# Kernel tuning notes

Measured on AMD Instinct MI355X. Metric: run time of the kernel, lower is better.

The kernel has to match this reference:

```python
import jax, jax.numpy as jnp
import numpy as np

N, M, E = 100000, 50000, 1600000
C_IN, C_OUT = 128, 128
BN_EPS = 1e-5


def setup_inputs() -> dict:
    key = jax.random.key(0)
    ks = jax.random.split(key, 10)
    ref_bxyz = jax.random.normal(ks[0], (N, 4), dtype=jnp.float32)
    ref_feat = jax.random.normal(ks[1], (N, C_IN), dtype=jnp.float32)
    query_bxyz = jax.random.normal(ks[2], (M, 4), dtype=jnp.float32)
    e_ref = jax.random.randint(ks[3], (E,), 0, N)
    e_query = jax.random.randint(ks[4], (E,), 0, M)
    # pos_encoder: Linear(3, C_OUT); mlp: Linear(C_IN, C_OUT); BatchNorm1d(C_OUT)
    W_pos = jax.random.normal(ks[5], (C_OUT, 3), dtype=jnp.float32) / np.sqrt(3.0)
    b_pos = jnp.zeros((C_OUT,), dtype=jnp.float32)
    W_mlp = jax.random.normal(ks[6], (C_OUT, C_IN), dtype=jnp.float32) / np.sqrt(C_IN)
    b_mlp = jnp.zeros((C_OUT,), dtype=jnp.float32)
    gamma = jnp.ones((C_OUT,), dtype=jnp.float32)
    beta = jnp.zeros((C_OUT,), dtype=jnp.float32)
    return {
        "ref_bxyz": ref_bxyz, "ref_feat": ref_feat, "query_bxyz": query_bxyz,
        "e_ref": e_ref, "e_query": e_query,
        "W_pos": W_pos, "b_pos": b_pos, "W_mlp": W_mlp, "b_mlp": b_mlp,
        "gamma": gamma, "beta": beta,
    }


def reference(ref_bxyz, ref_feat, query_bxyz, e_ref, e_query,
              W_pos, b_pos, W_mlp, b_mlp, gamma, beta):
    num_q = query_bxyz.shape[0]
    # gather endpoints, xyz difference (drop batch-index column 0)
    pos_diff = (ref_bxyz[e_ref] - query_bxyz[e_query])[:, 1:4]          # [E, 3]
    pos_embedding = pos_diff @ W_pos.T + b_pos                           # [E, C_OUT]
    output_feat = (ref_feat @ W_mlp.T + b_mlp)[e_ref]                   # [E, C_OUT]
    # scatter-mean into queries (empty segments -> 0, clamp count at 1)
    s = jax.ops.segment_sum(pos_embedding + output_feat, e_query, num_segments=num_q)
    cnt = jax.ops.segment_sum(jnp.ones((e_query.shape[0],), pos_embedding.dtype),
                              e_query, num_segments=num_q)
    query_feat = s / jnp.maximum(cnt, 1.0)[:, None]                     # [M, C_OUT]
    # BatchNorm1d (training-mode batch stats, biased variance) + ReLU
    mu = jnp.mean(query_feat, axis=0)
    var = jnp.mean(jnp.square(query_feat - mu), axis=0)
    normed = (query_feat - mu) * jax.lax.rsqrt(var + BN_EPS) * gamma + beta
    return jax.nn.relu(normed)
```

## Files before the change

### kernel.cpp

```cpp
#include <hip/hip_runtime.h>


__device__ __forceinline__ float bf_lo(unsigned u) {
  union { unsigned u; float f; } c; c.u = u << 16; return c.f;
}
__device__ __forceinline__ float bf_hi(unsigned u) {
  union { unsigned u; float f; } c; c.u = u & 0xFFFF0000u; return c.f;
}
__device__ __forceinline__ unsigned pack_bf(float x, float y) {
  union { float f; unsigned u; } a, b; a.f = x; b.f = y;
  unsigned lo = (a.u + 0x7FFFu + ((a.u >> 16) & 1u)) >> 16;
  unsigned hi = (b.u + 0x7FFFu + ((b.u >> 16) & 1u)) >> 16;
  return lo | (hi << 16);
}

__global__ __launch_bounds__(256) void k_build_cvt(
    const int* __restrict__ eq, const int* __restrict__ er,
    int* __restrict__ head, int2* __restrict__ node,
    const float4* __restrict__ featf, uint4* __restrict__ featb,
    int E_, int n8) {
  int i = blockIdx.x * blockDim.x + threadIdx.x;
  if (i < n8) {
    float4 a = featf[2 * i], b = featf[2 * i + 1];
    uint4 o;
    o.x = pack_bf(a.x, a.y);
    o.y = pack_bf(a.z, a.w);
    o.z = pack_bf(b.x, b.y);
    o.w = pack_bf(b.z, b.w);
    featb[i] = o;
  }
  if (i < E_) {
    int q = eq[i];
    int prev = atomicExch(&head[q], i);
    node[i] = make_int2(prev, er[i]);
  }
}

__global__ __launch_bounds__(256) void k_accum_b(const int* __restrict__ head,
                                                 const int2* __restrict__ node,
                                                 const uint4* __restrict__ featb,
                                                 const float* __restrict__ bxyz,
                                                 float4* __restrict__ accF4,
                                                 float* __restrict__ possum, int M_) {
  int q = blockIdx.x * 16 + (threadIdx.x >> 4);
  int l = threadIdx.x & 15;
  if (q >= M_) return;
  int i = head[q];
  float a0 = 0.f, a1 = 0.f, a2 = 0.f, a3 = 0.f;
  float a4 = 0.f, a5 = 0.f, a6 = 0.f, a7 = 0.f;
  float p = 0.f, c = 0.f;
  while (i >= 0) {
    int2 nd = node[i];
    int r = nd.y;
    uint4 v = featb[(size_t)r * 16 + l];
    a0 += bf_lo(v.x); a1 += bf_hi(v.x);
    a2 += bf_lo(v.y); a3 += bf_hi(v.y);
    a4 += bf_lo(v.z); a5 += bf_hi(v.z);
    a6 += bf_lo(v.w); a7 += bf_hi(v.w);
    if (l < 3) p += bxyz[r * 4 + 1 + l];
    c += 1.f;
    i = nd.x;
  }
  float4 o0 = make_float4(a0, a1, a2, a3);
  float4 o1 = make_float4(a4, a5, a6, a7);
  accF4[(size_t)q * 32 + l * 2] = o0;
  accF4[(size_t)q * 32 + l * 2 + 1] = o1;
  if (l < 3) possum[q * 4 + l] = p;
  if (l == 3) possum[q * 4 + 3] = c;
}

__global__ __launch_bounds__(256) void k_gemm(
    const float* __restrict__ accF, const float4* __restrict__ possum4,
    const float* __restrict__ qxyz,
    const float* __restrict__ Wm, const float* __restrict__ Wp,
    const float* __restrict__ bm, const float* __restrict__ bp,
    float* __restrict__ out, float* __restrict__ stats, int M_) {
  __shared__ float sA[32 * 132];
  __shared__ float sW[128 * 34];
  int t = threadIdx.x;
  int q0 = blockIdx.x * 32;
  #pragma unroll
  for (int i = 0; i < 4; ++i) {
    int f = t + 256 * i;
    int q = f >> 5;
    int kk = (f & 31) << 2;
    float4 v = make_float4(0.f, 0.f, 0.f, 0.f);
    if (q0 + q < M_) v = *(const float4*)&accF[(q0 + q) * 128 + kk];
    *(float4*)&sA[q * 132 + kk] = v;
  }
  float acc[4][4];
  #pragma unroll
  for (int i = 0; i < 4; ++i)
    #pragma unroll
    for (int j = 0; j < 4; ++j) acc[i][j] = 0.f;
  int q0l = (t >> 5) << 2;
  int cb = t & 31;
  float2* sW2 = (float2*)sW;
  const float2* Wm2 = (const float2*)Wm;
  for (int kt = 0; kt < 4; ++kt) {
    __syncthreads();
    #pragma unroll
    for (int i = 0; i < 8; ++i) {
      int f = t + 256 * i;
      int c = f >> 4;
      int kk2 = f & 15;
      sW2[c * 17 + kk2] = Wm2[c * 64 + kt * 16 + kk2];
    }
    __syncthreads();
    #pragma unroll
    for (int kk4 = 0; kk4 < 8; ++kk4) {
      float4 av[4];
      float2 wa[4], wb[4];
      #pragma unroll
      for (int i = 0; i < 4; ++i)
        av[i] = *(const float4*)&sA[(q0l + i) * 132 + kt * 32 + (kk4 << 2)];
      #pragma unroll
      for (int j = 0; j < 4; ++j) {
        int c = cb + 32 * j;
        wa[j] = sW2[c * 17 + kk4 * 2];
        wb[j] = sW2[c * 17 + kk4 * 2 + 1];
      }
      #pragma unroll
      for (int i = 0; i < 4; ++i)
        #pragma unroll
        for (int j = 0; j < 4; ++j) {
          acc[i][j] = fmaf(av[i].x, wa[j].x, acc[i][j]);
          acc[i][j] = fmaf(av[i].y, wa[j].y, acc[i][j]);
          acc[i][j] = fmaf(av[i].z, wb[j].x, acc[i][j]);
          acc[i][j] = fmaf(av[i].w, wb[j].y, acc[i][j]);
        }
    }
  }
  float fcnt[4], inv[4], dx[4], dy[4], dz[4];
  #pragma unroll
  for (int i = 0; i < 4; ++i) {
    int q = q0 + q0l + i;
    if (q < M_) {
      float4 ps = possum4[q];
      float fc = ps.w;
      fcnt[i] = fc;
      inv[i] = 1.f / fmaxf(fc, 1.f);
      dx[i] = ps.x - fc * qxyz[q * 4 + 1];
      dy[i] = ps.y - fc * qxyz[q * 4 + 2];
      dz[i] = ps.z - fc * qxyz[q * 4 + 3];
    } else {
      fcnt[i] = 0.f; inv[i] = 1.f; dx[i] = dy[i] = dz[i] = 0.f;
    }
  }
  float psum[4], psq[4];
  #pragma unroll
  for (int j = 0; j < 4; ++j) {
    int c = cb + 32 * j;
    float w0 = Wp[c * 3 + 0], w1 = Wp[c * 3 + 1], w2 = Wp[c * 3 + 2];
    float bb = bm[c] + bp[c];
    float s = 0.f, s2 = 0.f;
    #pragma unroll
    for (int i = 0; i < 4; ++i) {
      int q = q0 + q0l + i;
      float v = acc[i][j] + dx[i] * w0 + dy[i] * w1 + dz[i] * w2 + fcnt[i] * bb;
      float val = v * inv[i];
      if (q >= M_) val = 0.f;
      if (q < M_) out[q * 128 + c] = val;
      s += val; s2 += val * val;
    }
    psum[j] = s; psq[j] = s2;
  }
  __syncthreads();
  float* red = sA;
  int rg = t >> 5;
  #pragma unroll
  for (int j = 0; j < 4; ++j) {
    int c = cb + 32 * j;
    red[c * 8 + rg] = psum[j];
    red[1024 + c * 8 + rg] = psq[j];
  }
  __syncthreads();
  if (t < 128) {
    float s = 0.f, s2 = 0.f;
    #pragma unroll
    for (int r = 0; r < 8; ++r) {
      s += red[t * 8 + r];
      s2 += red[1024 + t * 8 + r];
    }
    atomicAdd(&stats[t], s);
    atomicAdd(&stats[128 + t], s2);
  }
}

__global__ __launch_bounds__(256) void k_bnapply(float* __restrict__ out,
                                                 const float* __restrict__ stats,
                                                 const float* __restrict__ gamma,
                                                 const float* __restrict__ beta,
                                                 float inv_m, int total4) {
  __shared__ float sc[128], sh[128];
  int t = threadIdx.x;
  if (t < 128) {
    float mu = stats[t] * inv_m;
    float var = stats[128 + t] * inv_m - mu * mu;
    var = fmaxf(var, 0.f);
    float s = gamma[t] * rsqrtf(var + 1e-5f);
    sc[t] = s;
    sh[t] = beta[t] - mu * s;
  }
  __syncthreads();
  const float4* sc4 = (const float4*)sc;
  const float4* sh4 = (const float4*)sh;
  float4* o4 = (float4*)out;
  for (int i = blockIdx.x * blockDim.x + t; i < total4;
       i += gridDim.x * blockDim.x) {
    float4 v = o4[i];
    float4 s = sc4[i & 31];
    float4 h = sh4[i & 31];
    v.x = fmaxf(fmaf(v.x, s.x, h.x), 0.f);
    v.y = fmaxf(fmaf(v.y, s.y, h.y), 0.f);
    v.z = fmaxf(fmaf(v.z, s.z, h.z), 0.f);
    v.w = fmaxf(fmaf(v.w, s.w, h.w), 0.f);
    o4[i] = v;
  }
}

static inline size_t align256(size_t x) { return (x + 255) & ~(size_t)255; }

extern "C" void kernel_launch(void* const* d_in, const int* in_sizes, int n_in,
                              void* d_out, int out_size, void* d_ws, size_t ws_size,
                              hipStream_t stream) {
  const float* ref_bxyz   = (const float*)d_in[0];
  const float* ref_feat   = (const float*)d_in[1];
  const float* query_bxyz = (const float*)d_in[2];
  const int*   e_ref      = (const int*)d_in[3];
  const int*   e_query    = (const int*)d_in[4];
  const float* W_pos      = (const float*)d_in[5];
  const float* b_pos      = (const float*)d_in[6];
  const float* W_mlp      = (const float*)d_in[7];
  const float* b_mlp      = (const float*)d_in[8];
  const float* gamma      = (const float*)d_in[9];
  const float* beta       = (const float*)d_in[10];

  int N_ = in_sizes[0] / 4;
  int M_ = in_sizes[2] / 4;
  int E_ = in_sizes[3];

  char* ws = (char*)d_ws;
  size_t off = 0;
  int*   head   = (int*)(ws + off);   off += align256((size_t)M_ * 4);
  int2*  node   = (int2*)(ws + off);  off += align256((size_t)E_ * 8);
  float* possum = (float*)(ws + off); off += align256((size_t)M_ * 4 * 4);
  float* accF   = (float*)(ws + off); off += align256((size_t)M_ * 128 * 4);
  float* stats  = (float*)(ws + off); off += align256(2 * 128 * 4);
  uint4* featb  = (uint4*)(ws + off);

  hipMemsetAsync(head, 0xFF, (size_t)M_ * 4, stream);
  hipMemsetAsync(stats, 0, 2 * 128 * 4, stream);

  float* out = (float*)d_out;
  int n8 = N_ * 16;
  int nwork = (E_ > n8) ? E_ : n8;

  k_build_cvt<<<(nwork + 255) / 256, 256, 0, stream>>>(
      e_query, e_ref, head, node, (const float4*)ref_feat, featb, E_, n8);
  k_accum_b<<<(M_ + 15) / 16, 256, 0, stream>>>(head, node, featb, ref_bxyz,
                                                (float4*)accF, possum, M_);
  k_gemm<<<(M_ + 31) / 32, 256, 0, stream>>>(accF, (const float4*)possum, query_bxyz,
                                             W_mlp, W_pos, b_mlp, b_pos, out, stats, M_);
  k_bnapply<<<2048, 256, 0, stream>>>(out, stats, gamma, beta, 1.f / (float)M_,
                                      M_ * 32);
}
```

Baseline: 353.1 us.

## Fuse gather-accumulate into GEMM kernel, keeping sums in shared memory

Merges the per-query linked-list gather/accumulate kernel into the GEMM kernel, so each block accumulates its 32 queries directly into shared memory instead of writing and re-reading a 25 MB fp32 accumulator buffer. Each half-wave walks two query lists at once to expose more memory-level parallelism. The stats memset moves into the build kernel, and the BN-apply grid is halved. The cost is GEMM work serialized behind irregular list walks within a block, plus a higher occupancy target from launch_bounds(256,4).

```diff
diff --git a/kernel.cpp b/kernel.cpp
--- a/kernel.cpp
+++ b/kernel.cpp
@@ -18,8 +18,9 @@
     const int* __restrict__ eq, const int* __restrict__ er,
     int* __restrict__ head, int2* __restrict__ node,
     const float4* __restrict__ featf, uint4* __restrict__ featb,
-    int E_, int n8) {
+    float* __restrict__ stats, int E_, int n8) {
   int i = blockIdx.x * blockDim.x + threadIdx.x;
+  if (i < 256) stats[i] = 0.f;
   if (i < n8) {
     float4 a = featf[2 * i], b = featf[2 * i + 1];
     uint4 o;
@@ -36,58 +37,55 @@
   }
 }
 
-__global__ __launch_bounds__(256) void k_accum_b(const int* __restrict__ head,
-                                                 const int2* __restrict__ node,
-                                                 const uint4* __restrict__ featb,
-                                                 const float* __restrict__ bxyz,
-                                                 float4* __restrict__ accF4,
-                                                 float* __restrict__ possum, int M_) {
-  int q = blockIdx.x * 16 + (threadIdx.x >> 4);
-  int l = threadIdx.x & 15;
-  if (q >= M_) return;
-  int i = head[q];
-  float a0 = 0.f, a1 = 0.f, a2 = 0.f, a3 = 0.f;
-  float a4 = 0.f, a5 = 0.f, a6 = 0.f, a7 = 0.f;
-  float p = 0.f, c = 0.f;
-  while (i >= 0) {
-    int2 nd = node[i];
-    int r = nd.y;
-    uint4 v = featb[(size_t)r * 16 + l];
-    a0 += bf_lo(v.x); a1 += bf_hi(v.x);
-    a2 += bf_lo(v.y); a3 += bf_hi(v.y);
-    a4 += bf_lo(v.z); a5 += bf_hi(v.z);
-    a6 += bf_lo(v.w); a7 += bf_hi(v.w);
-    if (l < 3) p += bxyz[r * 4 + 1 + l];
-    c += 1.f;
-    i = nd.x;
-  }
-  float4 o0 = make_float4(a0, a1, a2, a3);
-  float4 o1 = make_float4(a4, a5, a6, a7);
-  accF4[(size_t)q * 32 + l * 2] = o0;
-  accF4[(size_t)q * 32 + l * 2 + 1] = o1;
-  if (l < 3) possum[q * 4 + l] = p;
-  if (l == 3) possum[q * 4 + 3] = c;
-}
-
-__global__ __launch_bounds__(256) void k_gemm(
-    const float* __restrict__ accF, const float4* __restrict__ possum4,
+__global__ __launch_bounds__(256, 4) void k_fused(
+    const int* __restrict__ head, const int2* __restrict__ node,
+    const uint4* __restrict__ featb, const float* __restrict__ bxyz,
     const float* __restrict__ qxyz,
     const float* __restrict__ Wm, const float* __restrict__ Wp,
     const float* __restrict__ bm, const float* __restrict__ bp,
     float* __restrict__ out, float* __restrict__ stats, int M_) {
   __shared__ float sA[32 * 132];
   __shared__ float sW[128 * 34];
+  __shared__ float sPS[32][4];
   int t = threadIdx.x;
   int q0 = blockIdx.x * 32;
-  #pragma unroll
-  for (int i = 0; i < 4; ++i) {
-    int f = t + 256 * i;
-    int q = f >> 5;
-    int kk = (f & 31) << 2;
-    float4 v = make_float4(0.f, 0.f, 0.f, 0.f);
-    if (q0 + q < M_) v = *(const float4*)&accF[(q0 + q) * 128 + kk];
-    *(float4*)&sA[q * 132 + kk] = v;
-  }
+  int hw = t >> 4, l = t & 15;
+
+  {
+    int qa = q0 + hw, qb = q0 + hw + 16;
+    int ia = (qa < M_) ? head[qa] : -1;
+    int ib = (qb < M_) ? head[qb] : -1;
+    float aA0=0.f,aA1=0.f,aA2=0.f,aA3=0.f,aA4=0.f,aA5=0.f,aA6=0.f,aA7=0.f;
+    float aB0=0.f,aB1=0.f,aB2=0.f,aB3=0.f,aB4=0.f,aB5=0.f,aB6=0.f,aB7=0.f;
+    float pA=0.f,cA=0.f,pB=0.f,cB=0.f;
+    while (ia >= 0 || ib >= 0) {
+      bool da = ia >= 0, db = ib >= 0;
+      int2 na, nb; uint4 va, vb;
+      if (da) na = node[ia];
+      if (db) nb = node[ib];
+      if (da) va = featb[(size_t)na.y * 16 + l];
+      if (db) vb = featb[(size_t)nb.y * 16 + l];
+      if (da) {
+        aA0+=bf_lo(va.x); aA1+=bf_hi(va.x); aA2+=bf_lo(va.y); aA3+=bf_hi(va.y);
+        aA4+=bf_lo(va.z); aA5+=bf_hi(va.z); aA6+=bf_lo(va.w); aA7+=bf_hi(va.w);
+        if (l < 3) pA += bxyz[na.y * 4 + 1 + l];
+        cA += 1.f; ia = na.x;
+      }
+      if (db) {
+        aB0+=bf_lo(vb.x); aB1+=bf_hi(vb.x); aB2+=bf_lo(vb.y); aB3+=bf_hi(vb.y);
+        aB4+=bf_lo(vb.z); aB5+=bf_hi(vb.z); aB6+=bf_lo(vb.w); aB7+=bf_hi(vb.w);
+        if (l < 3) pB += bxyz[nb.y * 4 + 1 + l];
+        cB += 1.f; ib = nb.x;
+      }
+    }
+    *(float4*)&sA[hw * 132 + 8 * l]          = make_float4(aA0,aA1,aA2,aA3);
+    *(float4*)&sA[hw * 132 + 8 * l + 4]      = make_float4(aA4,aA5,aA6,aA7);
+    *(float4*)&sA[(hw + 16) * 132 + 8 * l]     = make_float4(aB0,aB1,aB2,aB3);
+    *(float4*)&sA[(hw + 16) * 132 + 8 * l + 4] = make_float4(aB4,aB5,aB6,aB7);
+    if (l < 3) { sPS[hw][l] = pA; sPS[hw + 16][l] = pB; }
+    if (l == 3) { sPS[hw][3] = cA; sPS[hw + 16][3] = cB; }
+  }
+
   float acc[4][4];
   #pragma unroll
   for (int i = 0; i < 4; ++i)
@@ -134,15 +132,15 @@
   float fcnt[4], inv[4], dx[4], dy[4], dz[4];
   #pragma unroll
   for (int i = 0; i < 4; ++i) {
-    int q = q0 + q0l + i;
+    int row = q0l + i;
+    int q = q0 + row;
     if (q < M_) {
-      float4 ps = possum4[q];
-      float fc = ps.w;
+      float fc = sPS[row][3];
       fcnt[i] = fc;
       inv[i] = 1.f / fmaxf(fc, 1.f);
-      dx[i] = ps.x - fc * qxyz[q * 4 + 1];
-      dy[i] = ps.y - fc * qxyz[q * 4 + 2];
-      dz[i] = ps.z - fc * qxyz[q * 4 + 3];
+      dx[i] = sPS[row][0] - fc * qxyz[q * 4 + 1];
+      dy[i] = sPS[row][1] - fc * qxyz[q * 4 + 2];
+      dz[i] = sPS[row][2] - fc * qxyz[q * 4 + 3];
     } else {
       fcnt[i] = 0.f; inv[i] = 1.f; dx[i] = dy[i] = dz[i] = 0.f;
     }
@@ -244,24 +242,20 @@
   size_t off = 0;
   int*   head   = (int*)(ws + off);   off += align256((size_t)M_ * 4);
   int2*  node   = (int2*)(ws + off);  off += align256((size_t)E_ * 8);
-  float* possum = (float*)(ws + off); off += align256((size_t)M_ * 4 * 4);
-  float* accF   = (float*)(ws + off); off += align256((size_t)M_ * 128 * 4);
   float* stats  = (float*)(ws + off); off += align256(2 * 128 * 4);
   uint4* featb  = (uint4*)(ws + off);
 
   hipMemsetAsync(head, 0xFF, (size_t)M_ * 4, stream);
-  hipMemsetAsync(stats, 0, 2 * 128 * 4, stream);
 
   float* out = (float*)d_out;
   int n8 = N_ * 16;
   int nwork = (E_ > n8) ? E_ : n8;
 
   k_build_cvt<<<(nwork + 255) / 256, 256, 0, stream>>>(
-      e_query, e_ref, head, node, (const float4*)ref_feat, featb, E_, n8);
-  k_accum_b<<<(M_ + 15) / 16, 256, 0, stream>>>(head, node, featb, ref_bxyz,
-                                                (float4*)accF, possum, M_);
-  k_gemm<<<(M_ + 31) / 32, 256, 0, stream>>>(accF, (const float4*)possum, query_bxyz,
-                                             W_mlp, W_pos, b_mlp, b_pos, out, stats, M_);
-  k_bnapply<<<2048, 256, 0, stream>>>(out, stats, gamma, beta, 1.f / (float)M_,
+      e_query, e_ref, head, node, (const float4*)ref_feat, featb, stats, E_, n8);
+  k_fused<<<(M_ + 31) / 32, 256, 0, stream>>>(head, node, featb, ref_bxyz,
+                                              query_bxyz, W_mlp, W_pos, b_mlp,
+                                              b_pos, out, stats, M_);
+  k_bnapply<<<1024, 256, 0, stream>>>(out, stats, gamma, beta, 1.f / (float)M_,
                                       M_ * 32);
 }
```

After: 396.4 us. +12.3%, slower.

## Fuse pipeline into one cooperative persistent kernel with grid syncs

Applied to the files above, without the earlier changes.

Replaces the two memsets and four separate kernel launches with a single cooperative kernel. The kernel runs the init, bf16 conversion and linked-list build, gather-accumulate, GEMM with BN stats, and BN apply as phases separated by grid.sync, using grid-stride loops sized to occupancy. This removes launch gaps and memset overhead. In exchange it caps parallelism at the resident-block count, adds grid-wide barriers, and changes GEMM tiling (smaller W slice per k-step). A fallback path keeps the multi-kernel launch if the cooperative launch fails.

```diff
diff --git a/kernel.cpp b/kernel.cpp
--- a/kernel.cpp
+++ b/kernel.cpp
@@ -1,4 +1,7 @@
 #include <hip/hip_runtime.h>
+#include <hip/hip_cooperative_groups.h>
+
+namespace cg = cooperative_groups;
 
 
 __device__ __forceinline__ float bf_lo(unsigned u) {
@@ -14,12 +17,235 @@
   return lo | (hi << 16);
 }
 
+struct P {
+  const int* eq; const int* er;
+  int* head; int2* node;
+  const float4* featf; uint4* featb;
+  const float* bxyz; const float* qxyz;
+  const float* Wm; const float* Wp; const float* bm; const float* bp;
+  const float* gamma; const float* beta;
+  float* out; float* stats; float4* accF4; float* possum;
+  int M, E, n8; float inv_m;
+};
+
+__global__ __launch_bounds__(256, 6) void k_all(P p) {
+  cg::grid_group grid = cg::this_grid();
+  __shared__ float sA[32 * 132];
+  __shared__ float sW[128 * 18];
+  __shared__ float sPS[32][4];
+  int t = threadIdx.x;
+  int nb = gridDim.x;
+  int gtid = blockIdx.x * 256 + t;
+  int gsz = nb * 256;
+
+  for (int i = gtid; i < p.M; i += gsz) p.head[i] = -1;
+  if (gtid < 256) p.stats[gtid] = 0.f;
+  grid.sync();
+
+  for (int i = gtid; i < p.n8; i += gsz) {
+    float4 a = p.featf[2 * i], b = p.featf[2 * i + 1];
+    uint4 o;
+    o.x = pack_bf(a.x, a.y);
+    o.y = pack_bf(a.z, a.w);
+    o.z = pack_bf(b.x, b.y);
+    o.w = pack_bf(b.z, b.w);
+    p.featb[i] = o;
+  }
+  for (int i = gtid; i < p.E; i += gsz) {
+    int q = p.eq[i];
+    int prev = atomicExch(&p.head[q], i);
+    p.node[i] = make_int2(prev, p.er[i]);
+  }
+  __threadfence();
+  grid.sync();
+
+  {
+    int grp = gtid >> 4, l = gtid & 15, ngrp = gsz >> 4;
+    for (int q = grp; q < p.M; q += ngrp) {
+      int i = p.head[q];
+      float a0=0.f,a1=0.f,a2=0.f,a3=0.f,a4=0.f,a5=0.f,a6=0.f,a7=0.f;
+      float ps = 0.f, c = 0.f;
+      while (i >= 0) {
+        int2 nd = p.node[i];
+        int r = nd.y;
+        uint4 v = p.featb[(size_t)r * 16 + l];
+        a0 += bf_lo(v.x); a1 += bf_hi(v.x);
+        a2 += bf_lo(v.y); a3 += bf_hi(v.y);
+        a4 += bf_lo(v.z); a5 += bf_hi(v.z);
+        a6 += bf_lo(v.w); a7 += bf_hi(v.w);
+        if (l < 3) ps += p.bxyz[r * 4 + 1 + l];
+        c += 1.f;
+        i = nd.x;
+      }
+      p.accF4[(size_t)q * 32 + 2 * l]     = make_float4(a0, a1, a2, a3);
+      p.accF4[(size_t)q * 32 + 2 * l + 1] = make_float4(a4, a5, a6, a7);
+      if (l < 3) p.possum[q * 4 + l] = ps;
+      if (l == 3) p.possum[q * 4 + 3] = c;
+    }
+  }
+  __threadfence();
+  grid.sync();
+
+  {
+    const float* accF = (const float*)p.accF4;
+    const float4* possum4 = (const float4*)p.possum;
+    int ntile = (p.M + 31) / 32;
+    int q0l = (t >> 5) << 2;
+    int cb = t & 31;
+    float2* sW2 = (float2*)sW;
+    const float2* Wm2 = (const float2*)p.Wm;
+    for (int tile = blockIdx.x; tile < ntile; tile += nb) {
+      int q0 = tile * 32;
+      #pragma unroll
+      for (int i = 0; i < 4; ++i) {
+        int f = t + 256 * i;
+        int q = f >> 5;
+        int kk = (f & 31) << 2;
+        float4 v = make_float4(0.f, 0.f, 0.f, 0.f);
+        if (q0 + q < p.M) v = *(const float4*)&accF[(size_t)(q0 + q) * 128 + kk];
+        *(float4*)&sA[q * 132 + kk] = v;
+      }
+      if (t < 32) {
+        float4 ps = make_float4(0.f, 0.f, 0.f, 0.f);
+        if (q0 + t < p.M) ps = possum4[q0 + t];
+        sPS[t][0] = ps.x; sPS[t][1] = ps.y; sPS[t][2] = ps.z; sPS[t][3] = ps.w;
+      }
+      float acc[4][4];
+      #pragma unroll
+      for (int i = 0; i < 4; ++i)
+        #pragma unroll
+        for (int j = 0; j < 4; ++j) acc[i][j] = 0.f;
+      for (int kt = 0; kt < 8; ++kt) {
+        __syncthreads();
+        #pragma unroll
+        for (int i = 0; i < 4; ++i) {
+          int f = t + 256 * i;
+          int c = f >> 3;
+          int kk2 = f & 7;
+          sW2[c * 9 + kk2] = Wm2[c * 64 + kt * 8 + kk2];
+        }
+        __syncthreads();
+        #pragma unroll
+        for (int kk4 = 0; kk4 < 4; ++kk4) {
+          float4 av[4];
+          float2 wa[4], wb[4];
+          #pragma unroll
+          for (int i = 0; i < 4; ++i)
+            av[i] = *(const float4*)&sA[(q0l + i) * 132 + kt * 16 + (kk4 << 2)];
+          #pragma unroll
+          for (int j = 0; j < 4; ++j) {
+            int c = cb + 32 * j;
+            wa[j] = sW2[c * 9 + kk4 * 2];
+            wb[j] = sW2[c * 9 + kk4 * 2 + 1];
+          }
+          #pragma unroll
+          for (int i = 0; i < 4; ++i)
+            #pragma unroll
+            for (int j = 0; j < 4; ++j) {
+              acc[i][j] = fmaf(av[i].x, wa[j].x, acc[i][j]);
+              acc[i][j] = fmaf(av[i].y, wa[j].y, acc[i][j]);
+              acc[i][j] = fmaf(av[i].z, wb[j].x, acc[i][j]);
+              acc[i][j] = fmaf(av[i].w, wb[j].y, acc[i][j]);
+            }
+        }
+      }
+      float fcnt[4], inv[4], dx[4], dy[4], dz[4];
+      #pragma unroll
+      for (int i = 0; i < 4; ++i) {
+        int row = q0l + i;
+        int q = q0 + row;
+        if (q < p.M) {
+          float fc = sPS[row][3];
+          fcnt[i] = fc;
+          inv[i] = 1.f / fmaxf(fc, 1.f);
+          dx[i] = sPS[row][0] - fc * p.qxyz[q * 4 + 1];
+          dy[i] = sPS[row][1] - fc * p.qxyz[q * 4 + 2];
+          dz[i] = sPS[row][2] - fc * p.qxyz[q * 4 + 3];
+        } else {
+          fcnt[i] = 0.f; inv[i] = 1.f; dx[i] = dy[i] = dz[i] = 0.f;
+        }
+      }
+      float psum[4], psq[4];
+      #pragma unroll
+      for (int j = 0; j < 4; ++j) {
+        int c = cb + 32 * j;
+        float w0 = p.Wp[c * 3 + 0], w1 = p.Wp[c * 3 + 1], w2 = p.Wp[c * 3 + 2];
+        float bb = p.bm[c] + p.bp[c];
+        float s = 0.f, s2 = 0.f;
+        #pragma unroll
+        for (int i = 0; i < 4; ++i) {
+          int q = q0 + q0l + i;
+          float v = acc[i][j] + dx[i] * w0 + dy[i] * w1 + dz[i] * w2 + fcnt[i] * bb;
+          float val = v * inv[i];
+          if (q >= p.M) val = 0.f;
+          if (q < p.M) p.out[(size_t)q * 128 + c] = val;
+          s += val; s2 += val * val;
+        }
+        psum[j] = s; psq[j] = s2;
+      }
+      __syncthreads();
+      float* red = sA;
+      int rg = t >> 5;
+      #pragma unroll
+      for (int j = 0; j < 4; ++j) {
+        int c = cb + 32 * j;
+        red[c * 8 + rg] = psum[j];
+        red[1024 + c * 8 + rg] = psq[j];
+      }
+      __syncthreads();
+      if (t < 128) {
+        float s = 0.f, s2 = 0.f;
+        #pragma unroll
+        for (int r = 0; r < 8; ++r) {
+          s += red[t * 8 + r];
+          s2 += red[1024 + t * 8 + r];
+        }
+        atomicAdd(&p.stats[t], s);
+        atomicAdd(&p.stats[128 + t], s2);
+      }
+      __syncthreads();
+    }
+  }
+  __threadfence();
+  grid.sync();
+
+  {
+    float* sc = sW;
+    float* sh = sW + 128;
+    if (t < 128) {
+      float mu = p.stats[t] * p.inv_m;
+      float var = p.stats[128 + t] * p.inv_m - mu * mu;
+      var = fmaxf(var, 0.f);
+      float s = p.gamma[t] * rsqrtf(var + 1e-5f);
+      sc[t] = s;
+      sh[t] = p.beta[t] - mu * s;
+    }
+    __syncthreads();
+    const float4* sc4 = (const float4*)sc;
+    const float4* sh4 = (const float4*)sh;
+    float4* o4 = (float4*)p.out;
+    int total4 = p.M * 32;
+    for (int i = gtid; i < total4; i += gsz) {
+      float4 v = o4[i];
+      float4 s = sc4[i & 31];
+      float4 h = sh4[i & 31];
+      v.x = fmaxf(fmaf(v.x, s.x, h.x), 0.f);
+      v.y = fmaxf(fmaf(v.y, s.y, h.y), 0.f);
+      v.z = fmaxf(fmaf(v.z, s.z, h.z), 0.f);
+      v.w = fmaxf(fmaf(v.w, s.w, h.w), 0.f);
+      o4[i] = v;
+    }
+  }
+}
+
+
 __global__ __launch_bounds__(256) void k_build_cvt(
     const int* __restrict__ eq, const int* __restrict__ er,
     int* __restrict__ head, int2* __restrict__ node,
     const float4* __restrict__ featf, uint4* __restrict__ featb,
-    int E_, int n8) {
+    float* __restrict__ stats, int E_, int n8) {
   int i = blockIdx.x * blockDim.x + threadIdx.x;
+  if (i < 256) stats[i] = 0.f;
   if (i < n8) {
     float4 a = featf[2 * i], b = featf[2 * i + 1];
     uint4 o;
@@ -46,9 +272,8 @@
   int l = threadIdx.x & 15;
   if (q >= M_) return;
   int i = head[q];
-  float a0 = 0.f, a1 = 0.f, a2 = 0.f, a3 = 0.f;
-  float a4 = 0.f, a5 = 0.f, a6 = 0.f, a7 = 0.f;
-  float p = 0.f, c = 0.f;
+  float a0=0.f,a1=0.f,a2=0.f,a3=0.f,a4=0.f,a5=0.f,a6=0.f,a7=0.f;
+  float ps = 0.f, c = 0.f;
   while (i >= 0) {
     int2 nd = node[i];
     int r = nd.y;
@@ -57,15 +282,13 @@
     a2 += bf_lo(v.y); a3 += bf_hi(v.y);
     a4 += bf_lo(v.z); a5 += bf_hi(v.z);
     a6 += bf_lo(v.w); a7 += bf_hi(v.w);
-    if (l < 3) p += bxyz[r * 4 + 1 + l];
+    if (l < 3) ps += bxyz[r * 4 + 1 + l];
     c += 1.f;
     i = nd.x;
   }
-  float4 o0 = make_float4(a0, a1, a2, a3);
-  float4 o1 = make_float4(a4, a5, a6, a7);
-  accF4[(size_t)q * 32 + l * 2] = o0;
-  accF4[(size_t)q * 32 + l * 2 + 1] = o1;
-  if (l < 3) possum[q * 4 + l] = p;
+  accF4[(size_t)q * 32 + 2 * l]     = make_float4(a0, a1, a2, a3);
+  accF4[(size_t)q * 32 + 2 * l + 1] = make_float4(a4, a5, a6, a7);
+  if (l < 3) possum[q * 4 + l] = ps;
   if (l == 3) possum[q * 4 + 3] = c;
 }
 
@@ -244,24 +467,43 @@
   size_t off = 0;
   int*   head   = (int*)(ws + off);   off += align256((size_t)M_ * 4);
   int2*  node   = (int2*)(ws + off);  off += align256((size_t)E_ * 8);
+  float* stats  = (float*)(ws + off); off += align256(2 * 128 * 4);
   float* possum = (float*)(ws + off); off += align256((size_t)M_ * 4 * 4);
   float* accF   = (float*)(ws + off); off += align256((size_t)M_ * 128 * 4);
-  float* stats  = (float*)(ws + off); off += align256(2 * 128 * 4);
   uint4* featb  = (uint4*)(ws + off);
-
-  hipMemsetAsync(head, 0xFF, (size_t)M_ * 4, stream);
-  hipMemsetAsync(stats, 0, 2 * 128 * 4, stream);
 
   float* out = (float*)d_out;
   int n8 = N_ * 16;
-  int nwork = (E_ > n8) ? E_ : n8;
-
-  k_build_cvt<<<(nwork + 255) / 256, 256, 0, stream>>>(
-      e_query, e_ref, head, node, (const float4*)ref_feat, featb, E_, n8);
-  k_accum_b<<<(M_ + 15) / 16, 256, 0, stream>>>(head, node, featb, ref_bxyz,
-                                                (float4*)accF, possum, M_);
-  k_gemm<<<(M_ + 31) / 32, 256, 0, stream>>>(accF, (const float4*)possum, query_bxyz,
-                                             W_mlp, W_pos, b_mlp, b_pos, out, stats, M_);
-  k_bnapply<<<2048, 256, 0, stream>>>(out, stats, gamma, beta, 1.f / (float)M_,
-                                      M_ * 32);
-}
+
+  P p;
+  p.eq = e_query; p.er = e_ref; p.head = head; p.node = node;
+  p.featf = (const float4*)ref_feat; p.featb = featb;
+  p.bxyz = ref_bxyz; p.qxyz = query_bxyz;
+  p.Wm = W_mlp; p.Wp = W_pos; p.bm = b_mlp; p.bp = b_pos;
+  p.gamma = gamma; p.beta = beta;
+  p.out = out; p.stats = stats; p.accF4 = (float4*)accF; p.possum = possum;
+  p.M = M_; p.E = E_; p.n8 = n8; p.inv_m = 1.f / (float)M_;
+
+  int numCU = 256, maxb = 0;
+  hipDeviceGetAttribute(&numCU, hipDeviceAttributeMultiprocessorCount, 0);
+  hipError_t oe = hipOccupancyMaxActiveBlocksPerMultiprocessor(&maxb, k_all, 256, 0);
+  if (oe != hipSuccess || maxb < 1) maxb = 4;
+  int grid = numCU * maxb;
+
+  void* args[] = { (void*)&p };
+  hipError_t err = hipLaunchCooperativeKernel((void*)k_all, dim3(grid), dim3(256),
+                                              args, 0, stream);
+  if (err != hipSuccess) {
+    int nwork = (E_ > n8) ? E_ : n8;
+    hipMemsetAsync(head, 0xFF, (size_t)M_ * 4, stream);
+    k_build_cvt<<<(nwork + 255) / 256, 256, 0, stream>>>(
+        e_query, e_ref, head, node, (const float4*)ref_feat, featb, stats, E_, n8);
+    k_accum_b<<<(M_ + 15) / 16, 256, 0, stream>>>(head, node, featb, ref_bxyz,
+                                                  (float4*)accF, possum, M_);
+    k_gemm<<<(M_ + 31) / 32, 256, 0, stream>>>(accF, (const float4*)possum,
+                                               query_bxyz, W_mlp, W_pos, b_mlp,
+                                               b_pos, out, stats, M_);
+    k_bnapply<<<1024, 256, 0, stream>>>(out, stats, gamma, beta, 1.f / (float)M_,
+                                        M_ * 32);
+  }
+}
```

Result: slower. 1.017 ms (+187.9%).

## Split per-query linked lists into four heads to cut atomic contention

Applied to the files above, without the earlier changes.

Each query now has four linked-list heads, selected by edge index mod 4. This spreads the atomicExch traffic during list building and shortens each serial pointer chase in the accumulation kernel. The stats zeroing moves from a memset into the build kernel, and the BN-apply grid is halved. The cost is a larger head array to memset and four sequential list walks per query.

```diff
diff --git a/kernel.cpp b/kernel.cpp
--- a/kernel.cpp
+++ b/kernel.cpp
@@ -16,10 +16,11 @@
 
 __global__ __launch_bounds__(256) void k_build_cvt(
     const int* __restrict__ eq, const int* __restrict__ er,
-    int* __restrict__ head, int2* __restrict__ node,
+    int* __restrict__ head4, int2* __restrict__ node,
     const float4* __restrict__ featf, uint4* __restrict__ featb,
-    int E_, int n8) {
+    float* __restrict__ stats, int E_, int n8) {
   int i = blockIdx.x * blockDim.x + threadIdx.x;
+  if (i < 256) stats[i] = 0.f;
   if (i < n8) {
     float4 a = featf[2 * i], b = featf[2 * i + 1];
     uint4 o;
@@ -31,12 +32,12 @@
   }
   if (i < E_) {
     int q = eq[i];
-    int prev = atomicExch(&head[q], i);
+    int prev = atomicExch(&head4[4 * q + (i & 3)], i);
     node[i] = make_int2(prev, er[i]);
   }
 }
 
-__global__ __launch_bounds__(256) void k_accum_b(const int* __restrict__ head,
+__global__ __launch_bounds__(256) void k_accum_b(const int* __restrict__ head4,
                                                  const int2* __restrict__ node,
                                                  const uint4* __restrict__ featb,
                                                  const float* __restrict__ bxyz,
@@ -45,27 +46,27 @@
   int q = blockIdx.x * 16 + (threadIdx.x >> 4);
   int l = threadIdx.x & 15;
   if (q >= M_) return;
-  int i = head[q];
-  float a0 = 0.f, a1 = 0.f, a2 = 0.f, a3 = 0.f;
-  float a4 = 0.f, a5 = 0.f, a6 = 0.f, a7 = 0.f;
-  float p = 0.f, c = 0.f;
-  while (i >= 0) {
-    int2 nd = node[i];
-    int r = nd.y;
-    uint4 v = featb[(size_t)r * 16 + l];
-    a0 += bf_lo(v.x); a1 += bf_hi(v.x);
-    a2 += bf_lo(v.y); a3 += bf_hi(v.y);
-    a4 += bf_lo(v.z); a5 += bf_hi(v.z);
-    a6 += bf_lo(v.w); a7 += bf_hi(v.w);
-    if (l < 3) p += bxyz[r * 4 + 1 + l];
-    c += 1.f;
-    i = nd.x;
-  }
-  float4 o0 = make_float4(a0, a1, a2, a3);
-  float4 o1 = make_float4(a4, a5, a6, a7);
-  accF4[(size_t)q * 32 + l * 2] = o0;
-  accF4[(size_t)q * 32 + l * 2 + 1] = o1;
-  if (l < 3) possum[q * 4 + l] = p;
+  float a0=0.f,a1=0.f,a2=0.f,a3=0.f,a4=0.f,a5=0.f,a6=0.f,a7=0.f;
+  float ps = 0.f, c = 0.f;
+  #pragma unroll
+  for (int s = 0; s < 4; ++s) {
+    int i = head4[4 * q + s];
+    while (i >= 0) {
+      int2 nd = node[i];
+      int r = nd.y;
+      uint4 v = featb[(size_t)r * 16 + l];
+      a0 += bf_lo(v.x); a1 += bf_hi(v.x);
+      a2 += bf_lo(v.y); a3 += bf_hi(v.y);
+      a4 += bf_lo(v.z); a5 += bf_hi(v.z);
+      a6 += bf_lo(v.w); a7 += bf_hi(v.w);
+      if (l < 3) ps += bxyz[r * 4 + 1 + l];
+      c += 1.f;
+      i = nd.x;
+    }
+  }
+  accF4[(size_t)q * 32 + 2 * l]     = make_float4(a0, a1, a2, a3);
+  accF4[(size_t)q * 32 + 2 * l + 1] = make_float4(a4, a5, a6, a7);
+  if (l < 3) possum[q * 4 + l] = ps;
   if (l == 3) possum[q * 4 + 3] = c;
 }
 
@@ -242,26 +243,26 @@
 
   char* ws = (char*)d_ws;
   size_t off = 0;
-  int*   head   = (int*)(ws + off);   off += align256((size_t)M_ * 4);
+  int*   head4  = (int*)(ws + off);   off += align256((size_t)M_ * 4 * 4);
   int2*  node   = (int2*)(ws + off);  off += align256((size_t)E_ * 8);
+  float* stats  = (float*)(ws + off); off += align256(2 * 128 * 4);
   float* possum = (float*)(ws + off); off += align256((size_t)M_ * 4 * 4);
   float* accF   = (float*)(ws + off); off += align256((size_t)M_ * 128 * 4);
-  float* stats  = (float*)(ws + off); off += align256(2 * 128 * 4);
   uint4* featb  = (uint4*)(ws + off);
 
-  hipMemsetAsync(head, 0xFF, (size_t)M_ * 4, stream);
-  hipMemsetAsync(stats, 0, 2 * 128 * 4, stream);
+  hipMemsetAsync(head4, 0xFF, (size_t)M_ * 4 * 4, stream);
 
   float* out = (float*)d_out;
   int n8 = N_ * 16;
   int nwork = (E_ > n8) ? E_ : n8;
 
   k_build_cvt<<<(nwork + 255) / 256, 256, 0, stream>>>(
-      e_query, e_ref, head, node, (const float4*)ref_feat, featb, E_, n8);
-  k_accum_b<<<(M_ + 15) / 16, 256, 0, stream>>>(head, node, featb, ref_bxyz,
+      e_query, e_ref, head4, node, (const float4*)ref_feat, featb, stats, E_, n8);
+  k_accum_b<<<(M_ + 15) / 16, 256, 0, stream>>>(head4, node, featb, ref_bxyz,
                                                 (float4*)accF, possum, M_);
-  k_gemm<<<(M_ + 31) / 32, 256, 0, stream>>>(accF, (const float4*)possum, query_bxyz,
-                                             W_mlp, W_pos, b_mlp, b_pos, out, stats, M_);
-  k_bnapply<<<2048, 256, 0, stream>>>(out, stats, gamma, beta, 1.f / (float)M_,
+  k_gemm<<<(M_ + 31) / 32, 256, 0, stream>>>(accF, (const float4*)possum,
+                                             query_bxyz, W_mlp, W_pos, b_mlp,
+                                             b_pos, out, stats, M_);
+  k_bnapply<<<1024, 256, 0, stream>>>(out, stats, gamma, beta, 1.f / (float)M_,
                                       M_ * 32);
 }
```

Result: no change. 350.7 us (-0.7%).
